# Kernel optimization log

Hardware: AMD Instinct MI355X
Metric: run time of the kernel (lower is better)

## Reference

```python
import jax, jax.numpy as jnp
import numpy as np

V, H, L, B, S = 32000, 1024, 2, 32, 512

def setup_inputs() -> dict:
    key = jax.random.key(0)
    ks = jax.random.split(key, 24)
    g = lambda k, shp, s=0.02: jax.random.normal(k, shp, dtype=jnp.float32) * s
    inp = {
        'input_ids': jax.random.randint(ks[0], (1, B), 0, V),
        'hidden': jax.random.normal(ks[1], (L, B, H), dtype=jnp.float32),
        'encoder_output': jax.random.normal(ks[2], (S, B, H), dtype=jnp.float32),
        'encoder_output_pinyin': jax.random.normal(ks[3], (S, B, H), dtype=jnp.float32),
        'embedding': g(ks[4], (V, H), 1.0),
        'W_ih0': g(ks[5], (3 * H, H)), 'W_hh0': g(ks[6], (3 * H, H)),
        'b_ih0': jnp.zeros((3 * H,), jnp.float32), 'b_hh0': jnp.zeros((3 * H,), jnp.float32),
        'W_ih1': g(ks[7], (3 * H, H)), 'W_hh1': g(ks[8], (3 * H, H)),
        'b_ih1': jnp.zeros((3 * H,), jnp.float32), 'b_hh1': jnp.zeros((3 * H,), jnp.float32),
        'att_fc1_w': g(ks[9], (H, 3 * H)), 'att_fc1_b': jnp.zeros((H,), jnp.float32),
        'att_fc2_w': g(ks[10], (1, H)), 'att_fc2_b': jnp.zeros((1,), jnp.float32),
        'attp_fc1_w': g(ks[11], (H, 3 * H)), 'attp_fc1_b': jnp.zeros((H,), jnp.float32),
        'attp_fc2_w': g(ks[12], (1, H)), 'attp_fc2_b': jnp.zeros((1,), jnp.float32),
        'attn_fc_w': g(ks[13], (H, 3 * H)), 'attn_fc_b': jnp.zeros((H,), jnp.float32),
        'fc_w': g(ks[14], (V, H)), 'fc_b': jnp.zeros((V,), jnp.float32),
    }
    return inp


def _gru_cell(x, h, Wih, Whh, bih, bhh):
    # torch GRU gate order: r, z, n
    gi = x @ Wih.T + bih          # [B, 3H]
    gh = h @ Whh.T + bhh          # [B, 3H]
    ir, iz, in_ = jnp.split(gi, 3, axis=-1)
    hr, hz, hn = jnp.split(gh, 3, axis=-1)
    r = jax.nn.sigmoid(ir + hr)
    z = jax.nn.sigmoid(iz + hz)
    n = jnp.tanh(in_ + r * hn)
    return (1.0 - z) * n + z * h


def _attention(hidden, enc, fc1_w, fc1_b, fc2_w, fc2_b):
    # hidden: [L, B, H], enc: [S, B, H]
    s, b = enc.shape[0], enc.shape[1]
    state = jnp.transpose(hidden, (1, 0, 2)).reshape(b, -1)       # [B, L*H]
    enc_b = jnp.transpose(enc, (1, 0, 2))                          # [B, S, H]
    state_rep = jnp.broadcast_to(state[:, None, :], (b, s, state.shape[-1]))
    concat = jnp.concatenate([state_rep, enc_b], axis=-1)          # [B, S, 3H]
    energy = jnp.tanh(concat @ fc1_w.T + fc1_b)                    # [B, S, H]
    energy = (energy @ fc2_w.T + fc2_b).transpose(0, 2, 1)         # [B, 1, S]
    alpha = jax.nn.softmax(energy, axis=2)
    context = jnp.einsum('bis,bsh->bih', alpha, enc_b)             # [B, 1, H]
    return jnp.transpose(context, (1, 0, 2)), alpha                # [1, B, H]


def reference(input_ids, hidden, encoder_output, encoder_output_pinyin, embedding,
              W_ih0, W_hh0, b_ih0, b_hh0, W_ih1, W_hh1, b_ih1, b_hh1,
              att_fc1_w, att_fc1_b, att_fc2_w, att_fc2_b,
              attp_fc1_w, attp_fc1_b, attp_fc2_w, attp_fc2_b,
              attn_fc_w, attn_fc_b, fc_w, fc_b):
    embedded = embedding[input_ids]             # [1, B, H] (dropout: eval mode = identity)
    x = embedded[0]                             # [B, H]
    h0 = _gru_cell(x, hidden[0], W_ih0, W_hh0, b_ih0, b_hh0)
    h1 = _gru_cell(h0, hidden[1], W_ih1, W_hh1, b_ih1, b_hh1)
    new_hidden = jnp.stack([h0, h1], axis=0)    # [L, B, H]
    output = h1[None]                           # [1, B, H]
    context, _ = _attention(new_hidden, encoder_output, att_fc1_w, att_fc1_b, att_fc2_w, att_fc2_b)
    context_p, _ = _attention(new_hidden, encoder_output_pinyin, attp_fc1_w, attp_fc1_b, attp_fc2_w, attp_fc2_b)
    fused = jnp.concatenate([output, context, context_p], axis=2)  # [1, B, 3H]
    output = jax.nn.relu(fused @ attn_fc_w.T + attn_fc_b)          # [1, B, H]
    logits = output @ fc_w.T + fc_b                                # [1, B, V]
    return logits, new_hidden
```

## Files before the change

### kernel.cpp

```cpp
#include <hip/hip_runtime.h>
#include <math.h>

#define Bsz 32
#define Hd  1024
#define Sd  512
#define Vd  32000

typedef __attribute__((ext_vector_type(8))) short v8s;
typedef __attribute__((ext_vector_type(4))) float v4f;

__device__ __forceinline__ float sigf(float x){ return 1.0f/(1.0f+__expf(-x)); }
__device__ __forceinline__ float ftanh(float x){
  float e = __expf(2.0f*x);
  return 1.0f - 2.0f/(e+1.0f);
}
__device__ __forceinline__ unsigned pk(float lo, float hi){
  return __builtin_amdgcn_perm(__float_as_uint(hi), __float_as_uint(lo), 0x07060302u);
}

__global__ void k_cvt_fc1w(const float* __restrict__ aw, const float* __restrict__ pw,
                           ushort* __restrict__ ab, ushort* __restrict__ pb){
  int tt = blockIdx.x*256 + threadIdx.x;
  int idx = tt*8;
  int s = idx >> 20;
  int r = idx & 1048575;
  int j = r >> 10, k = r & 1023;
  const float* src = (s? pw : aw) + (size_t)j*3072 + 2048 + k;
  float4 f0 = *(const float4*)src, f1 = *(const float4*)(src+4);
  uint4 p = { pk(f0.x,f0.y), pk(f0.z,f0.w), pk(f1.x,f1.y), pk(f1.z,f1.w) };
  *(uint4*)((s? pb : ab) + r) = p;
}

__global__ void k_embed(const int* __restrict__ ids, const float* __restrict__ emb,
                        float* __restrict__ x){
  int t = blockIdx.x*256 + threadIdx.x;
  int b = t >> 10, k = t & (Hd-1);
  x[t] = emb[(size_t)ids[b]*Hd + k];
}

__global__ void k_gates9(const float* __restrict__ x, const float* __restrict__ hid,
                         const float* __restrict__ Wih0, const float* __restrict__ Whh0,
                         const float* __restrict__ Whh1, float* __restrict__ gA){
  int blk = blockIdx.x;
  int g  = blk >> 9;
  int kc = (blk >> 7) & 3;
  int tt = (blk & 127)*256 + threadIdx.x;
  int b = tt & 31, j = tt >> 5;
  const float* vec; const float* w;
  if (g < 3){ vec = x + b*Hd; w = Wih0 + ((size_t)(g*Hd + j))*Hd; }
  else if (g < 6){ vec = hid + b*Hd; w = Whh0 + ((size_t)((g-3)*Hd + j))*Hd; }
  else { vec = hid + Bsz*Hd + b*Hd; w = Whh1 + ((size_t)((g-6)*Hd + j))*Hd; }
  const float4* v4 = (const float4*)(vec + kc*256);
  const float4* w4 = (const float4*)(w + kc*256);
  float acc = 0.f;
  #pragma unroll 8
  for (int k=0;k<64;k++){ float4 a=v4[k], ww=w4[k];
    acc += a.x*ww.x+a.y*ww.y+a.z*ww.z+a.w*ww.w; }
  atomicAdd(&gA[(size_t)g*32768 + j*32 + b], acc);
}

__global__ void k_gates3(const float* __restrict__ h0, const float* __restrict__ Wih1,
                         float* __restrict__ gB){
  int blk = blockIdx.x;
  int g  = blk >> 9;
  int kc = (blk >> 7) & 3;
  int tt = (blk & 127)*256 + threadIdx.x;
  int b = tt & 31, j = tt >> 5;
  const float4* v4 = (const float4*)(h0 + b*Hd + kc*256);
  const float4* w4 = (const float4*)(Wih1 + ((size_t)(g*Hd + j))*Hd + kc*256);
  float acc = 0.f;
  #pragma unroll 8
  for (int k=0;k<64;k++){ float4 a=v4[k], ww=w4[k];
    acc += a.x*ww.x+a.y*ww.y+a.z*ww.z+a.w*ww.w; }
  atomicAdd(&gB[(size_t)g*32768 + j*32 + b], acc);
}

__global__ void k_gru_comb(const float* __restrict__ xg, const float* __restrict__ hg,
                           const float* __restrict__ h, const float* __restrict__ bih,
                           const float* __restrict__ bhh, float* __restrict__ hnew){
  int tt = blockIdx.x*256 + threadIdx.x;
  int b = tt & 31, j = tt >> 5;
  float ir = xg[tt], iz = xg[32768 + tt], in_ = xg[2*32768 + tt];
  float hr = hg[tt], hz = hg[32768 + tt], hn  = hg[2*32768 + tt];
  float r = sigf(ir + bih[j]      + hr + bhh[j]);
  float z = sigf(iz + bih[Hd+j]   + hz + bhh[Hd+j]);
  float n = ftanh(in_ + bih[2*Hd+j] + r*(hn + bhh[2*Hd+j]));
  hnew[(size_t)b*Hd + j] = (1.f-z)*n + z*h[(size_t)b*Hd + j];
}

__global__ void k_spsplit(const float* __restrict__ h0, const float* __restrict__ h1,
                          const float* __restrict__ afc1w, const float* __restrict__ pfc1w,
                          float* __restrict__ spa_, float* __restrict__ spp_){
  int blk = blockIdx.x;
  int s  = blk >> 9;
  int kc = (blk >> 7) & 3;
  int tt = (blk & 127)*256 + threadIdx.x;
  int b = tt & 31, j = tt >> 5;
  const float* w = (s? pfc1w : afc1w) + (size_t)j*3*Hd + kc*512;
  const float* vec = (kc < 2 ? h0 : h1) + b*Hd + (kc & 1)*512;
  const float4* v4 = (const float4*)vec;
  const float4* w4 = (const float4*)w;
  float acc = 0.f;
  #pragma unroll 8
  for (int k=0;k<128;k++){ float4 a=v4[k], ww=w4[k];
    acc += a.x*ww.x+a.y*ww.y+a.z*ww.z+a.w*ww.w; }
  atomicAdd((s? spp_ : spa_) + (size_t)b*Hd + j, acc);
}

__global__ __launch_bounds__(256, 4)
void k_att_mfma(const float* __restrict__ enc0, const float* __restrict__ enc1,
                const ushort* __restrict__ wb0, const ushort* __restrict__ wb1,
                const float* __restrict__ sp0, const float* __restrict__ sp1,
                const float* __restrict__ b10, const float* __restrict__ b11,
                const float* __restrict__ w20, const float* __restrict__ w21,
                float* __restrict__ e0, float* __restrict__ e1){
  const int flat = blockIdx.x + (blockIdx.y << 3) + (blockIdx.z << 10);
  const int xcd  = flat & 7;
  const int widx = flat >> 3;
  const int z    = widx >> 7;
  const int rem  = widx & 127;
  const int rowt = (xcd << 4) + (rem >> 3);
  const int colb = rem & 7;

  const float*  enc = z? enc1 : enc0;
  const ushort* wb  = z? wb1  : wb0;
  const float*  sp  = z? sp1  : sp0;
  const float*  b1  = z? b11  : b10;
  const float*  fc2 = z? w21  : w20;
  float* e = z? e1 : e0;
  __shared__ __align__(16) ushort As[128*72];
  __shared__ __align__(16) ushort Bs[128*72];
  const int t = threadIdx.x;
  const int lane = t & 63;
  const int w = t >> 6;
  const int wm = w >> 1, wn = w & 1;
  const int q = lane >> 4, c15 = lane & 15;
  const int row0 = rowt * 128;
  const int col0 = colb * 128;

  const int lrow = t >> 3, lkp = (t & 7)*8;
  const float* gA = enc + (size_t)(row0 + lrow)*Hd + lkp;
  const int brow = t >> 1, bkp = (t & 1)*32;
  const ushort* gB = wb + (size_t)(col0 + brow)*Hd + bkp;

  v4f acc[4][4];
  for (int mi=0;mi<4;mi++) for (int ni=0;ni<4;ni++) acc[mi][ni] = (v4f){0.f,0.f,0.f,0.f};

  for (int k0 = 0; k0 < Hd; k0 += 64){
    #pragma unroll
    for (int i = 0; i < 4; i++){
      const float* p = gA + (size_t)i*32*Hd + k0;
      float4 a0 = *(const float4*)p;
      float4 a1 = *(const float4*)(p+4);
      uint4 pa = { pk(a0.x,a0.y), pk(a0.z,a0.w), pk(a1.x,a1.y), pk(a1.z,a1.w) };
      *(uint4*)&As[(i*32 + lrow)*72 + lkp] = pa;
    }
    {
      const uint4* pb4 = (const uint4*)(gB + k0);
      uint4 b0_=pb4[0], b1_=pb4[1], b2_=pb4[2], b3_=pb4[3];
      uint4* d = (uint4*)&Bs[brow*72 + bkp];
      d[0]=b0_; d[1]=b1_; d[2]=b2_; d[3]=b3_;
    }
    __syncthreads();
    #pragma unroll
    for (int kk = 0; kk < 2; kk++){
      v8s af[4], bf[4];
      #pragma unroll
      for (int mi=0;mi<4;mi++)
        af[mi] = *(const v8s*)&As[(wm*64 + mi*16 + c15)*72 + kk*32 + q*8];
      #pragma unroll
      for (int ni=0;ni<4;ni++)
        bf[ni] = *(const v8s*)&Bs[(wn*64 + ni*16 + c15)*72 + kk*32 + q*8];
      #pragma unroll
      for (int mi=0;mi<4;mi++)
        #pragma unroll
        for (int ni=0;ni<4;ni++)
          acc[mi][ni] = __builtin_amdgcn_mfma_f32_16x16x32_bf16(af[mi], bf[ni], acc[mi][ni], 0, 0, 0);
    }
    __syncthreads();
  }

  #pragma unroll
  for (int mi=0;mi<4;mi++){
    float rs[4] = {0.f,0.f,0.f,0.f};
    #pragma unroll
    for (int ni=0;ni<4;ni++){
      int col = col0 + wn*64 + ni*16 + c15;
      float w2 = fc2[col];
      float bb1 = b1[col];
      int bb = (mi & 1) * 16;
      #pragma unroll
      for (int r=0;r<4;r++){
        int b = bb + q*4 + r;
        float xv = acc[mi][ni][r] + sp[(size_t)b*Hd + col] + bb1;
        rs[r] += w2 * ftanh(xv);
      }
    }
    #pragma unroll
    for (int r=0;r<4;r++){
      float v = rs[r];
      v += __shfl_xor(v, 1);
      v += __shfl_xor(v, 2);
      v += __shfl_xor(v, 4);
      v += __shfl_xor(v, 8);
      if (c15 == 0)
        atomicAdd(&e[row0 + wm*64 + mi*16 + q*4 + r], v);
    }
  }
}

__global__ void k_softmax(float* __restrict__ ea_, float* __restrict__ ep_){
  float* e = blockIdx.y ? ep_ : ea_;
  const int b = blockIdx.x, t = threadIdx.x;
  __shared__ float red[256];
  float v1 = e[t*Bsz + b], v2 = e[(t+256)*Bsz + b];
  red[t] = fmaxf(v1, v2);
  __syncthreads();
  for (int off=128; off; off>>=1){ if (t<off) red[t]=fmaxf(red[t],red[t+off]); __syncthreads(); }
  float m = red[0];
  __syncthreads();
  float e1 = __expf(v1-m), e2 = __expf(v2-m);
  red[t] = e1 + e2;
  __syncthreads();
  for (int off=128; off; off>>=1){ if (t<off) red[t]+=red[t+off]; __syncthreads(); }
  float inv = 1.0f/red[0];
  e[t*Bsz + b] = e1*inv;
  e[(t+256)*Bsz + b] = e2*inv;
}

__global__ void k_context(const float* __restrict__ ea_, const float* __restrict__ ep_,
                          const float* __restrict__ enc0, const float* __restrict__ enc1,
                          float* __restrict__ ctx0, float* __restrict__ ctx1){
  const int z = blockIdx.z;
  const float* alpha = z? ep_ : ea_;
  const float* enc   = z? enc1 : enc0;
  float* ctx         = z? ctx1 : ctx0;
  const int b = blockIdx.x, c = blockIdx.y, t = threadIdx.x;
  float4 acc = {0,0,0,0};
  for (int s = c*64; s < c*64 + 64; s++){
    float a = alpha[s*Bsz + b];
    float4 ev = *(const float4*)(enc + (size_t)(s*Bsz+b)*Hd + t*4);
    acc.x += a*ev.x; acc.y += a*ev.y; acc.z += a*ev.z; acc.w += a*ev.w;
  }
  float* p = ctx + (size_t)b*Hd + t*4;
  atomicAdd(p+0, acc.x); atomicAdd(p+1, acc.y);
  atomicAdd(p+2, acc.z); atomicAdd(p+3, acc.w);
}

__global__ void k_fcsplit(const float* __restrict__ h1, const float* __restrict__ ctx,
                          const float* __restrict__ ctxp, const float* __restrict__ W,
                          float* __restrict__ o1acc){
  int blk = blockIdx.x;
  int c = blk >> 7;
  int tt = (blk & 127)*256 + threadIdx.x;
  int b = tt & 31, j = tt >> 5;
  int seg = c >> 2, off = (c & 3)*256;
  const float* vec = (seg==0 ? h1 : (seg==1 ? ctx : ctxp)) + b*Hd + off;
  const float* w = W + (size_t)j*3*Hd + seg*Hd + off;
  const float4* v4 = (const float4*)vec;
  const float4* w4 = (const float4*)w;
  float acc = 0.f;
  #pragma unroll 8
  for (int k=0;k<64;k++){ float4 a=v4[k], ww=w4[k];
    acc += a.x*ww.x+a.y*ww.y+a.z*ww.z+a.w*ww.w; }
  atomicAdd(&o1acc[(size_t)j*32 + b], acc);
}

__global__ void k_o1comb(const float* __restrict__ o1acc, const float* __restrict__ bias,
                         ushort* __restrict__ o1b){
  int tt = blockIdx.x*256 + threadIdx.x;
  int b = tt & 31, j = tt >> 5;
  float acc = fmaxf(o1acc[tt] + bias[j], 0.f);
  o1b[(size_t)b*Hd + j] = (ushort)(__float_as_uint(acc) >> 16);
}

__global__ __launch_bounds__(512)
void k_logits(const ushort* __restrict__ o1b, const float* __restrict__ fcw,
              const float* __restrict__ fcb, float* __restrict__ lg){
  const int t = threadIdx.x;
  const int lane = t & 63, w = t >> 6;
  const int q = lane >> 4, c15 = lane & 15;
  const int v0 = blockIdx.x * 128;
  const int col = v0 + w*16 + c15;
  const float*  gB  = fcw + (size_t)col*Hd + q*8;
  const ushort* gA0 = o1b + (size_t)c15*Hd + q*8;
  const ushort* gA1 = o1b + (size_t)(16 + c15)*Hd + q*8;
  v4f acc[2] = {(v4f){0,0,0,0},(v4f){0,0,0,0}};
  #pragma unroll 4
  for (int k=0;k<Hd;k+=32){
    float4 f0 = *(const float4*)(gB + k);
    float4 f1 = *(const float4*)(gB + k + 4);
    uint4 p = { pk(f0.x,f0.y), pk(f0.z,f0.w), pk(f1.x,f1.y), pk(f1.z,f1.w) };
    v8s bfrag = *(const v8s*)&p;
    v8s a0 = *(const v8s*)(gA0 + k);
    v8s a1 = *(const v8s*)(gA1 + k);
    acc[0] = __builtin_amdgcn_mfma_f32_16x16x32_bf16(a0, bfrag, acc[0], 0, 0, 0);
    acc[1] = __builtin_amdgcn_mfma_f32_16x16x32_bf16(a1, bfrag, acc[1], 0, 0, 0);
  }
  float bias = fcb[col];
  #pragma unroll
  for (int mf=0;mf<2;mf++)
    #pragma unroll
    for (int r=0;r<4;r++){
      int b = mf*16 + q*4 + r;
      lg[(size_t)b*Vd + col] = acc[mf][r] + bias;
    }
}

extern "C" void kernel_launch(void* const* d_in, const int* in_sizes, int n_in,
                              void* d_out, int out_size, void* d_ws, size_t ws_size,
                              hipStream_t stream) {
  const int*   ids  = (const int*)  d_in[0];
  const float* hid  = (const float*)d_in[1];
  const float* enc  = (const float*)d_in[2];
  const float* encp = (const float*)d_in[3];
  const float* emb  = (const float*)d_in[4];
  const float* Wih0 = (const float*)d_in[5];
  const float* Whh0 = (const float*)d_in[6];
  const float* bih0 = (const float*)d_in[7];
  const float* bhh0 = (const float*)d_in[8];
  const float* Wih1 = (const float*)d_in[9];
  const float* Whh1 = (const float*)d_in[10];
  const float* bih1 = (const float*)d_in[11];
  const float* bhh1 = (const float*)d_in[12];
  const float* afc1w= (const float*)d_in[13];
  const float* afc1b= (const float*)d_in[14];
  const float* afc2w= (const float*)d_in[15];
  const float* pfc1w= (const float*)d_in[17];
  const float* pfc1b= (const float*)d_in[18];
  const float* pfc2w= (const float*)d_in[19];
  const float* nfcw = (const float*)d_in[21];
  const float* nfcb = (const float*)d_in[22];
  const float* fcw  = (const float*)d_in[23];
  const float* fcb  = (const float*)d_in[24];

  float* outp   = (float*)d_out;
  float* logits = outp;
  float* h0     = outp + (size_t)Bsz*Vd;
  float* h1     = h0 + Bsz*Hd;

  float* ws = (float*)d_ws;
  ushort* fc1wab = (ushort*)ws;
  ushort* fc1wpb = (ushort*)(ws + 524288);
  float* x    = ws + 1048576;
  float* spa  = ws + 1081344;
  float* spp  = ws + 1114112;
  float* ea   = ws + 1146880;
  float* ep   = ws + 1163264;
  float* ctx  = ws + 1179648;
  float* ctxp = ws + 1212416;
  float* gA   = ws + 1245184;
  float* gB   = ws + 1540096;
  float* o1a  = ws + 1638400;
  ushort* o1b = (ushort*)(ws + 1671168);

  hipMemsetAsync(spa, 0, (size_t)589824*sizeof(float), stream);

  k_cvt_fc1w<<<1024, 256, 0, stream>>>(afc1w, pfc1w, fc1wab, fc1wpb);
  k_embed   <<<Bsz*Hd/256, 256, 0, stream>>>(ids, emb, x);
  k_gates9  <<<4608, 256, 0, stream>>>(x, hid, Wih0, Whh0, Whh1, gA);
  k_gru_comb<<<128, 256, 0, stream>>>(gA, gA + 3*32768, hid, bih0, bhh0, h0);
  k_gates3  <<<1536, 256, 0, stream>>>(h0, Wih1, gB);
  k_gru_comb<<<128, 256, 0, stream>>>(gB, gA + 6*32768, hid + Bsz*Hd, bih1, bhh1, h1);
  k_spsplit <<<1024, 256, 0, stream>>>(h0, h1, afc1w, pfc1w, spa, spp);

  dim3 ga(Hd/128, Sd*Bsz/128, 2);
  k_att_mfma<<<ga, 256, 0, stream>>>(enc, encp, fc1wab, fc1wpb, spa, spp,
                                     afc1b, pfc1b, afc2w, pfc2w, ea, ep);

  k_softmax<<<dim3(Bsz,2), 256, 0, stream>>>(ea, ep);
  k_context<<<dim3(Bsz,8,2), 256, 0, stream>>>(ea, ep, enc, encp, ctx, ctxp);

  k_fcsplit<<<1536, 256, 0, stream>>>(h1, ctx, ctxp, nfcw, o1a);
  k_o1comb <<<128, 256, 0, stream>>>(o1a, nfcb, o1b);
  k_logits <<<Vd/128, 512, 0, stream>>>(o1b, fcw, fcb, logits);
}
```

Baseline: 911.5 us.

## Pre-convert encoder to swizzled bf16 tiles and stream via global_load_lds

```diff
diff --git a/kernel.cpp b/kernel.cpp
--- a/kernel.cpp
+++ b/kernel.cpp
@@ -9,6 +9,13 @@
 typedef __attribute__((ext_vector_type(8))) short v8s;
 typedef __attribute__((ext_vector_type(4))) float v4f;
 
+typedef __attribute__((address_space(1))) const unsigned int AS1c;
+typedef __attribute__((address_space(3))) unsigned int AS3u;
+
+__device__ __forceinline__ void gload16(const void* g, const ushort* l){
+  __builtin_amdgcn_global_load_lds((AS1c*)g, (AS3u*)l, 16, 0, 0);
+}
+
 __device__ __forceinline__ float sigf(float x){ return 1.0f/(1.0f+__expf(-x)); }
 __device__ __forceinline__ float ftanh(float x){
   float e = __expf(2.0f*x);
@@ -16,6 +23,35 @@
 }
 __device__ __forceinline__ unsigned pk(float lo, float hi){
   return __builtin_amdgcn_perm(__float_as_uint(hi), __float_as_uint(lo), 0x07060302u);
+}
+
+
+__global__ void k_cvt_fc1w_t(const float* __restrict__ aw, const float* __restrict__ pw,
+                             ushort* __restrict__ ab, ushort* __restrict__ pb){
+  int tt = blockIdx.x*256 + threadIdx.x;
+  int s = tt >> 17;
+  int j = (tt >> 7) & 1023;
+  int g = tt & 127;
+  const float* src = (s? pw : aw) + (size_t)j*3072 + 2048 + g*8;
+  float4 f0 = *(const float4*)src, f1 = *(const float4*)(src+4);
+  uint4 p = { pk(f0.x,f0.y), pk(f0.z,f0.w), pk(f1.x,f1.y), pk(f1.z,f1.w) };
+  int ct = j >> 7, cl = j & 127, kt = g >> 3, gl = g & 7;
+  size_t off = ((size_t)(ct*16 + kt))*8192 + (size_t)cl*64 + (((gl*8) ^ ((cl&7)<<3)));
+  *(uint4*)((s? pb : ab) + off) = p;
+}
+
+__global__ void k_cvt_enc(const float* __restrict__ e0, const float* __restrict__ e1,
+                          ushort* __restrict__ o0, ushort* __restrict__ o1){
+  int tt = blockIdx.x*256 + threadIdx.x;
+  int z = tt >> 21;
+  int r = (tt >> 7) & 16383;
+  int g = tt & 127;
+  const float* src = (z? e1 : e0) + (size_t)r*1024 + g*8;
+  float4 f0 = *(const float4*)src, f1 = *(const float4*)(src+4);
+  uint4 p = { pk(f0.x,f0.y), pk(f0.z,f0.w), pk(f1.x,f1.y), pk(f1.z,f1.w) };
+  int rt = r >> 7, rl = r & 127, kt = g >> 3, gl = g & 7;
+  size_t off = ((size_t)(rt*16 + kt))*8192 + (size_t)rl*64 + (((gl*8) ^ ((rl&7)<<3)));
+  *(uint4*)((z? o1 : o0) + off) = p;
 }
 
 __global__ void k_cvt_fc1w(const float* __restrict__ aw, const float* __restrict__ pw,
@@ -31,14 +67,8 @@
   *(uint4*)((s? pb : ab) + r) = p;
 }
 
-__global__ void k_embed(const int* __restrict__ ids, const float* __restrict__ emb,
-                        float* __restrict__ x){
-  int t = blockIdx.x*256 + threadIdx.x;
-  int b = t >> 10, k = t & (Hd-1);
-  x[t] = emb[(size_t)ids[b]*Hd + k];
-}
-
-__global__ void k_gates9(const float* __restrict__ x, const float* __restrict__ hid,
+__global__ void k_gates9(const int* __restrict__ ids, const float* __restrict__ emb,
+                         const float* __restrict__ hid,
                          const float* __restrict__ Wih0, const float* __restrict__ Whh0,
                          const float* __restrict__ Whh1, float* __restrict__ gA){
   int blk = blockIdx.x;
@@ -47,7 +77,7 @@
   int tt = (blk & 127)*256 + threadIdx.x;
   int b = tt & 31, j = tt >> 5;
   const float* vec; const float* w;
-  if (g < 3){ vec = x + b*Hd; w = Wih0 + ((size_t)(g*Hd + j))*Hd; }
+  if (g < 3){ vec = emb + (size_t)ids[b]*Hd; w = Wih0 + ((size_t)(g*Hd + j))*Hd; }
   else if (g < 6){ vec = hid + b*Hd; w = Whh0 + ((size_t)((g-3)*Hd + j))*Hd; }
   else { vec = hid + Bsz*Hd + b*Hd; w = Whh1 + ((size_t)((g-6)*Hd + j))*Hd; }
   const float4* v4 = (const float4*)(vec + kc*256);
@@ -108,6 +138,103 @@
 }
 
 __global__ __launch_bounds__(256, 4)
+void k_att_mfma2(const ushort* __restrict__ eb0, const ushort* __restrict__ eb1,
+                 const ushort* __restrict__ wb0, const ushort* __restrict__ wb1,
+                 const float* __restrict__ sp0, const float* __restrict__ sp1,
+                 const float* __restrict__ b10, const float* __restrict__ b11,
+                 const float* __restrict__ w20, const float* __restrict__ w21,
+                 float* __restrict__ e0, float* __restrict__ e1){
+  const int flat = blockIdx.x + (blockIdx.y << 3) + (blockIdx.z << 10);
+  const int xcd  = flat & 7;
+  const int widx = flat >> 3;
+  const int z    = widx >> 7;
+  const int rem  = widx & 127;
+  const int rowt = (xcd << 4) + (rem >> 3);
+  const int colb = rem & 7;
+
+  const ushort* eb = z? eb1 : eb0;
+  const ushort* wb = z? wb1 : wb0;
+  const float*  sp = z? sp1 : sp0;
+  const float*  b1 = z? b11 : b10;
+  const float*  fc2= z? w21 : w20;
+  float* e = z? e1 : e0;
+
+  __shared__ __align__(16) ushort As[128*64];
+  __shared__ __align__(16) ushort Bs[128*64];
+  const int t = threadIdx.x;
+  const int lane = t & 63;
+  const int w = t >> 6;
+  const int wm = w >> 1, wn = w & 1;
+  const int q = lane >> 4, c15 = lane & 15;
+  const int row0 = rowt * 128;
+  const int col0 = colb * 128;
+  const int rdk  = (c15 & 7) << 3;
+
+  const char* gAk = (const char*)(eb + (size_t)rowt*131072) + w*1024 + lane*16;
+  const char* gBk = (const char*)(wb + (size_t)colb*131072) + w*1024 + lane*16;
+
+  v4f acc[4][4];
+  #pragma unroll
+  for (int mi=0;mi<4;mi++)
+    #pragma unroll
+    for (int ni=0;ni<4;ni++) acc[mi][ni] = (v4f){0.f,0.f,0.f,0.f};
+
+  for (int kt = 0; kt < 16; kt++){
+    #pragma unroll
+    for (int j = 0; j < 4; j++){
+      gload16(gAk + j*4096, &As[j*2048 + w*512]);
+      gload16(gBk + j*4096, &Bs[j*2048 + w*512]);
+    }
+    __syncthreads();
+    #pragma unroll
+    for (int kk = 0; kk < 2; kk++){
+      v8s af[4], bf[4];
+      #pragma unroll
+      for (int mi=0;mi<4;mi++)
+        af[mi] = *(const v8s*)&As[(wm*64 + mi*16 + c15)*64 + ((kk*32 + q*8) ^ rdk)];
+      #pragma unroll
+      for (int ni=0;ni<4;ni++)
+        bf[ni] = *(const v8s*)&Bs[(wn*64 + ni*16 + c15)*64 + ((kk*32 + q*8) ^ rdk)];
+      #pragma unroll
+      for (int mi=0;mi<4;mi++)
+        #pragma unroll
+        for (int ni=0;ni<4;ni++)
+          acc[mi][ni] = __builtin_amdgcn_mfma_f32_16x16x32_bf16(af[mi], bf[ni], acc[mi][ni], 0, 0, 0);
+    }
+    __syncthreads();
+    gAk += 16384; gBk += 16384;
+  }
+
+  #pragma unroll
+  for (int mi=0;mi<4;mi++){
+    float rs[4] = {0.f,0.f,0.f,0.f};
+    #pragma unroll
+    for (int ni=0;ni<4;ni++){
+      int col = col0 + wn*64 + ni*16 + c15;
+      float w2 = fc2[col];
+      float bb1 = b1[col];
+      int bb = (mi & 1) * 16;
+      #pragma unroll
+      for (int r=0;r<4;r++){
+        int b = bb + q*4 + r;
+        float xv = acc[mi][ni][r] + sp[(size_t)b*Hd + col] + bb1;
+        rs[r] += w2 * ftanh(xv);
+      }
+    }
+    #pragma unroll
+    for (int r=0;r<4;r++){
+      float v = rs[r];
+      v += __shfl_xor(v, 1);
+      v += __shfl_xor(v, 2);
+      v += __shfl_xor(v, 4);
+      v += __shfl_xor(v, 8);
+      if (c15 == 0)
+        atomicAdd(&e[row0 + wm*64 + mi*16 + q*4 + r], v);
+    }
+  }
+}
+
+__global__ __launch_bounds__(256, 4)
 void k_att_mfma(const float* __restrict__ enc0, const float* __restrict__ enc1,
                 const ushort* __restrict__ wb0, const ushort* __restrict__ wb1,
                 const float* __restrict__ sp0, const float* __restrict__ sp1,
@@ -237,7 +364,9 @@
   float* ctx         = z? ctx1 : ctx0;
   const int b = blockIdx.x, c = blockIdx.y, t = threadIdx.x;
   float4 acc = {0,0,0,0};
-  for (int s = c*64; s < c*64 + 64; s++){
+  #pragma unroll
+  for (int i = 0; i < 16; i++){
+    int s = c*16 + i;
     float a = alpha[s*Bsz + b];
     float4 ev = *(const float4*)(enc + (size_t)(s*Bsz+b)*Hd + t*4);
     acc.x += a*ev.x; acc.y += a*ev.y; acc.z += a*ev.z; acc.w += a*ev.w;
@@ -286,7 +415,7 @@
   const ushort* gA0 = o1b + (size_t)c15*Hd + q*8;
   const ushort* gA1 = o1b + (size_t)(16 + c15)*Hd + q*8;
   v4f acc[2] = {(v4f){0,0,0,0},(v4f){0,0,0,0}};
-  #pragma unroll 4
+  #pragma unroll 8
   for (int k=0;k<Hd;k+=32){
     float4 f0 = *(const float4*)(gB + k);
     float4 f1 = *(const float4*)(gB + k + 4);
@@ -340,38 +469,76 @@
   float* h1     = h0 + Bsz*Hd;
 
   float* ws = (float*)d_ws;
-  ushort* fc1wab = (ushort*)ws;
-  ushort* fc1wpb = (ushort*)(ws + 524288);
-  float* x    = ws + 1048576;
-  float* spa  = ws + 1081344;
-  float* spp  = ws + 1114112;
-  float* ea   = ws + 1146880;
-  float* ep   = ws + 1163264;
-  float* ctx  = ws + 1179648;
-  float* ctxp = ws + 1212416;
-  float* gA   = ws + 1245184;
-  float* gB   = ws + 1540096;
-  float* o1a  = ws + 1638400;
-  ushort* o1b = (ushort*)(ws + 1671168);
-
-  hipMemsetAsync(spa, 0, (size_t)589824*sizeof(float), stream);
-
-  k_cvt_fc1w<<<1024, 256, 0, stream>>>(afc1w, pfc1w, fc1wab, fc1wpb);
-  k_embed   <<<Bsz*Hd/256, 256, 0, stream>>>(ids, emb, x);
-  k_gates9  <<<4608, 256, 0, stream>>>(x, hid, Wih0, Whh0, Whh1, gA);
-  k_gru_comb<<<128, 256, 0, stream>>>(gA, gA + 3*32768, hid, bih0, bhh0, h0);
-  k_gates3  <<<1536, 256, 0, stream>>>(h0, Wih1, gB);
-  k_gru_comb<<<128, 256, 0, stream>>>(gB, gA + 6*32768, hid + Bsz*Hd, bih1, bhh1, h1);
-  k_spsplit <<<1024, 256, 0, stream>>>(h0, h1, afc1w, pfc1w, spa, spp);
-
-  dim3 ga(Hd/128, Sd*Bsz/128, 2);
-  k_att_mfma<<<ga, 256, 0, stream>>>(enc, encp, fc1wab, fc1wpb, spa, spp,
-                                     afc1b, pfc1b, afc2w, pfc2w, ea, ep);
-
-  k_softmax<<<dim3(Bsz,2), 256, 0, stream>>>(ea, ep);
-  k_context<<<dim3(Bsz,8,2), 256, 0, stream>>>(ea, ep, enc, encp, ctx, ctxp);
-
-  k_fcsplit<<<1536, 256, 0, stream>>>(h1, ctx, ctxp, nfcw, o1a);
-  k_o1comb <<<128, 256, 0, stream>>>(o1a, nfcb, o1b);
-  k_logits <<<Vd/128, 512, 0, stream>>>(o1b, fcw, fcb, logits);
-}
+  const size_t NEED = (size_t)(17825792 + 589824 + 16384) * 4;
+
+  if (ws_size >= NEED){
+    ushort* fc1wab = (ushort*)ws;
+    ushort* fc1wpb = (ushort*)(ws + 524288);
+    ushort* eb0    = (ushort*)(ws + 1048576);
+    ushort* eb1    = (ushort*)(ws + 9437184);
+    float* spa  = ws + 17825792;
+    float* spp  = spa + 32768;
+    float* ea   = spa + 65536;
+    float* ep   = spa + 81920;
+    float* ctx  = spa + 98304;
+    float* ctxp = spa + 131072;
+    float* gA   = spa + 163840;
+    float* gB   = spa + 458752;
+    float* o1a  = spa + 557056;
+    ushort* o1b = (ushort*)(spa + 589824);
+
+    hipMemsetAsync(spa, 0, (size_t)589824*sizeof(float), stream);
+
+    k_cvt_fc1w_t<<<1024, 256, 0, stream>>>(afc1w, pfc1w, fc1wab, fc1wpb);
+    k_cvt_enc   <<<16384, 256, 0, stream>>>(enc, encp, eb0, eb1);
+    k_gates9    <<<4608, 256, 0, stream>>>(ids, emb, hid, Wih0, Whh0, Whh1, gA);
+    k_gru_comb  <<<128, 256, 0, stream>>>(gA, gA + 3*32768, hid, bih0, bhh0, h0);
+    k_gates3    <<<1536, 256, 0, stream>>>(h0, Wih1, gB);
+    k_gru_comb  <<<128, 256, 0, stream>>>(gB, gA + 6*32768, hid + Bsz*Hd, bih1, bhh1, h1);
+    k_spsplit   <<<1024, 256, 0, stream>>>(h0, h1, afc1w, pfc1w, spa, spp);
+
+    dim3 ga(Hd/128, Sd*Bsz/128, 2);
+    k_att_mfma2<<<ga, 256, 0, stream>>>(eb0, eb1, fc1wab, fc1wpb, spa, spp,
+                                        afc1b, pfc1b, afc2w, pfc2w, ea, ep);
+
+    k_softmax<<<dim3(Bsz,2), 256, 0, stream>>>(ea, ep);
+    k_context<<<dim3(Bsz,32,2), 256, 0, stream>>>(ea, ep, enc, encp, ctx, ctxp);
+
+    k_fcsplit<<<1536, 256, 0, stream>>>(h1, ctx, ctxp, nfcw, o1a);
+    k_o1comb <<<128, 256, 0, stream>>>(o1a, nfcb, o1b);
+    k_logits <<<Vd/128, 512, 0, stream>>>(o1b, fcw, fcb, logits);
+  } else {
+    ushort* fc1wab = (ushort*)ws;
+    ushort* fc1wpb = (ushort*)(ws + 524288);
+    float* spa  = ws + 1081344;
+    float* spp  = ws + 1114112;
+    float* ea   = ws + 1146880;
+    float* ep   = ws + 1163264;
+    float* ctx  = ws + 1179648;
+    float* ctxp = ws + 1212416;
+    float* gA   = ws + 1245184;
+    float* gB   = ws + 1540096;
+    float* o1a  = ws + 1638400;
+    ushort* o1b = (ushort*)(ws + 1671168);
+
+    hipMemsetAsync(spa, 0, (size_t)589824*sizeof(float), stream);
+
+    k_cvt_fc1w<<<1024, 256, 0, stream>>>(afc1w, pfc1w, fc1wab, fc1wpb);
+    k_gates9  <<<4608, 256, 0, stream>>>(ids, emb, hid, Wih0, Whh0, Whh1, gA);
+    k_gru_comb<<<128, 256, 0, stream>>>(gA, gA + 3*32768, hid, bih0, bhh0, h0);
+    k_gates3  <<<1536, 256, 0, stream>>>(h0, Wih1, gB);
+    k_gru_comb<<<128, 256, 0, stream>>>(gB, gA + 6*32768, hid + Bsz*Hd, bih1, bhh1, h1);
+    k_spsplit <<<1024, 256, 0, stream>>>(h0, h1, afc1w, pfc1w, spa, spp);
+
+    dim3 ga(Hd/128, Sd*Bsz/128, 2);
+    k_att_mfma<<<ga, 256, 0, stream>>>(enc, encp, fc1wab, fc1wpb, spa, spp,
+                                       afc1b, pfc1b, afc2w, pfc2w, ea, ep);
+
+    k_softmax<<<dim3(Bsz,2), 256, 0, stream>>>(ea, ep);
+    k_context<<<dim3(Bsz,32,2), 256, 0, stream>>>(ea, ep, enc, encp, ctx, ctxp);
+
+    k_fcsplit<<<1536, 256, 0, stream>>>(h1, ctx, ctxp, nfcw, o1a);
+    k_o1comb <<<128, 256, 0, stream>>>(o1a, nfcb, o1b);
+    k_logits <<<Vd/128, 512, 0, stream>>>(o1b, fcw, fcb, logits);
+  }
+}
```

New measurement: 898.0 us. Within noise of the previous version (-1.5%).
